# Optimization experiments

Measured on AMD Instinct MI355X. Metric: run time of the kernel, lower is better.

The kernel has to match this reference:

```python
import jax, jax.numpy as jnp
import numpy as np

B = 16384
D = 1024
NG = 64
H = 2  # num_heads = len(conv_kernel_sizes)


def setup_inputs() -> dict:
    key = jax.random.key(0)
    ks = jax.random.split(key, 12)
    s = 0.02
    return {
        "x": jax.random.normal(ks[0], (B, D), jnp.float32),
        "group_labels": jax.random.randint(ks[1], (B,), 0, NG, dtype=jnp.int32),
        "num_groups": NG,
        "conv_w2": jax.random.normal(ks[2], (2,), jnp.float32) * s,
        "conv_b2": jax.random.normal(ks[3], (), jnp.float32) * s,
        "conv_w4": jax.random.normal(ks[4], (4,), jnp.float32) * s,
        "conv_b4": jax.random.normal(ks[5], (), jnp.float32) * s,
        "intra_in_w": jax.random.normal(ks[6], (3 * D, D), jnp.float32) * s,
        "intra_in_b": jnp.zeros((3 * D,), jnp.float32),
        "intra_out_w": jax.random.normal(ks[7], (D, D), jnp.float32) * s,
        "intra_out_b": jnp.zeros((D,), jnp.float32),
        "inter_in_w": jax.random.normal(ks[8], (3 * D, D), jnp.float32) * s,
        "inter_in_b": jnp.zeros((3 * D,), jnp.float32),
        "inter_out_w": jax.random.normal(ks[9], (D, D), jnp.float32) * s,
        "inter_out_b": jnp.zeros((D,), jnp.float32),
        "lin_w": jax.random.normal(ks[10], (D, D), jnp.float32) * s,
        "lin_b": jnp.zeros((D,), jnp.float32),
    }


def _seg_conv(x_s, l_s, w, b):
    """Per-group Conv2d(1,1,(k,1),padding=(k//2,0)) along the group-sorted axis,
    with zero padding at group boundaries and output trimmed to group size.
    out[i] = sum_j w[j] * x[i + j - k//2] if same group else 0."""
    n = x_s.shape[0]
    k = w.shape[0]
    pad = k // 2
    xp = jnp.pad(x_s, ((pad, pad), (0, 0)))
    lp = jnp.pad(l_s, (pad, pad), constant_values=-1)
    out = jnp.zeros_like(x_s)
    for j in range(k):  # k <= 4, static
        m = (lp[j:j + n] == l_s)[:, None]
        out = out + w[j] * jnp.where(m, xp[j:j + n], 0.0)
    return out + b


def _mha_self(xs, in_w, in_b, out_w, out_b, h):
    """torch nn.MultiheadAttention self-attention, seq-first xs: [S, N, D]."""
    S, N, Dm = xs.shape
    dh = Dm // h
    qkv = jnp.einsum('snd,ed->sne', xs, in_w) + in_b
    q, k, v = jnp.split(qkv, 3, axis=-1)
    q = q.reshape(S, N, h, dh)
    k = k.reshape(S, N, h, dh)
    v = v.reshape(S, N, h, dh)
    scores = jnp.einsum('qnhd,knhd->nhqk', q, k) / np.float32(np.sqrt(dh))
    a = jax.nn.softmax(scores, axis=-1)
    o = jnp.einsum('nhqk,knhd->qnhd', a, v).reshape(S, N, Dm)
    return jnp.einsum('snd,ed->sne', o, out_w) + out_b


def reference(x, group_labels, num_groups, conv_w2, conv_b2, conv_w4, conv_b4,
              intra_in_w, intra_in_b, intra_out_w, intra_out_b,
              inter_in_w, inter_in_b, inter_out_w, inter_out_b, lin_w, lin_b):
    n, d = x.shape
    labels = group_labels.astype(jnp.int32)
    perm = jnp.argsort(labels)  # stable: preserves original order within groups
    x_s = x[perm]
    l_s = labels[perm]

    # per-group convs -> [2, N, D] token stack (seq-first for MHA)
    t2 = _seg_conv(x_s, l_s, conv_w2, conv_b2)
    t4 = _seg_conv(x_s, l_s, conv_w4, conv_b4)
    tok = jnp.stack([t2, t4], axis=0)

    # intra attention over the 2 conv tokens per position, mean, then Linear
    intra = _mha_self(tok, intra_in_w, intra_in_b, intra_out_w, intra_out_b, H).mean(axis=0)
    lin_out = intra @ lin_w.T + lin_b  # [N, D]

    # inter-group: seq-len-1 attention over FIRST row of each other group ==
    # out_proj(v_proj(first_row)); mean over the other present groups.
    counts = jax.ops.segment_sum(jnp.ones((n,), jnp.int32), labels, num_segments=num_groups)
    present = counts > 0
    first_idx = jax.ops.segment_min(jnp.arange(n), labels, num_segments=num_groups)
    first_rows = x[jnp.where(present, first_idx, 0)]  # [NG, D]
    Wv = inter_in_w[2 * d:]
    bv = inter_in_b[2 * d:]
    f = (first_rows @ Wv.T + bv) @ inter_out_w.T + inter_out_b  # [NG, D]
    f = jnp.where(present[:, None], f, 0.0)
    n_present = jnp.sum(present.astype(jnp.int32))
    denom = jnp.maximum(n_present - 1, 1).astype(x.dtype)
    inter_mean = (jnp.sum(f, axis=0)[None, :] - f) / denom
    inter_mean = inter_mean * (n_present > 1).astype(x.dtype)

    out_s = lin_out + inter_mean[l_s]
    return jnp.zeros_like(x).at[perm].set(out_s)
```

## Files before the change

### kernel.cpp

```cpp
#include <hip/hip_runtime.h>
#include <hip/hip_bf16.h>

#define B_N 16384
#define D_DIM 1024
#define NGRP 64
#define NCHUNK 64
#define CHUNK 256

typedef __attribute__((ext_vector_type(8))) short short8;
typedef __attribute__((ext_vector_type(8))) unsigned short ushort8;
typedef __attribute__((ext_vector_type(4))) unsigned short ushort4v;
typedef __attribute__((ext_vector_type(4))) float floatx4;

__device__ __forceinline__ float bf2f(unsigned short h) {
    union { unsigned u; float f; } c; c.u = ((unsigned)h) << 16; return c.f;
}
__device__ __forceinline__ unsigned short f2bf(float f) {
    union { float f; unsigned u; } c; c.f = f;
    unsigned r = c.u + 0x7FFFu + ((c.u >> 16) & 1u);
    return (unsigned short)(r >> 16);
}

__device__ __forceinline__ void gload_lds16(const void* g, void* l) {
    __builtin_amdgcn_global_load_lds(
        (const __attribute__((address_space(1))) unsigned int*)g,
        (__attribute__((address_space(3))) unsigned int*)l, 16, 0, 0);
}

__global__ __launch_bounds__(256) void k_hist(const int* __restrict__ labels,
                                              int* __restrict__ hist) {
    __shared__ int lh[NGRP];
    int t = threadIdx.x, c = blockIdx.x;
    if (t < NGRP) lh[t] = 0;
    __syncthreads();
    int lab = labels[c * CHUNK + t];
    atomicAdd(&lh[lab], 1);
    __syncthreads();
    if (t < NGRP) hist[c * NGRP + t] = lh[t];
}

__global__ void k_scan(int* __restrict__ hist, int* __restrict__ gstart,
                       int* __restrict__ counts, float* __restrict__ scal) {
    __shared__ int cnt[NGRP];
    __shared__ int st[NGRP + 1];
    int g = threadIdx.x;
    int run = 0;
    for (int c = 0; c < NCHUNK; c++) {
        int v = hist[c * NGRP + g];
        hist[c * NGRP + g] = run;
        run += v;
    }
    cnt[g] = run;
    counts[g] = run;
    __syncthreads();
    if (g == 0) {
        int s = 0, np = 0;
        for (int i = 0; i < NGRP; i++) { st[i] = s; s += cnt[i]; np += (cnt[i] > 0); }
        st[NGRP] = s;
        scal[0] = (np > 1) ? 1.0f / (float)(np - 1) : 0.0f;
    }
    __syncthreads();
    gstart[g] = st[g];
    if (g == 0) gstart[NGRP] = st[NGRP];
    for (int c = 0; c < NCHUNK; c++) hist[c * NGRP + g] += st[g];
}

__global__ __launch_bounds__(256) void k_scatter(const int* __restrict__ labels,
                                                 const int* __restrict__ hist,
                                                 int* __restrict__ perm,
                                                 int* __restrict__ ls) {
    __shared__ int lab[CHUNK];
    int c = blockIdx.x, t = threadIdx.x;
    int i = c * CHUNK + t;
    int L = labels[i];
    lab[t] = L;
    __syncthreads();
    int rank = 0;
    for (int j = 0; j < t; j++) rank += (lab[j] == L);
    int pos = hist[c * NGRP + L] + rank;
    perm[pos] = i;
    ls[pos] = L;
}

__global__ __launch_bounds__(256) void k_conv(const float* __restrict__ x,
                                              const int* __restrict__ perm,
                                              const int* __restrict__ ls,
                                              const float* __restrict__ w2, const float* __restrict__ b2,
                                              const float* __restrict__ w4, const float* __restrict__ b4,
                                              unsigned short* __restrict__ tok, int c0, int Bc) {
    const int il = blockIdx.x;
    const int i = c0 + il;
    const int li = ls[i];
    const int p0 = perm[i];
    const int pm1 = (i >= 1 && ls[i - 1] == li) ? perm[i - 1] : -1;
    const int pm2 = (i >= 2 && ls[i - 2] == li) ? perm[i - 2] : -1;
    const int pp1 = (i + 1 < B_N && ls[i + 1] == li) ? perm[i + 1] : -1;
    const int c = threadIdx.x * 4;
    floatx4 z = (floatx4)0.0f;
    floatx4 x0 = *(const floatx4*)(x + (size_t)p0 * D_DIM + c);
    floatx4 xm1 = (pm1 >= 0) ? *(const floatx4*)(x + (size_t)pm1 * D_DIM + c) : z;
    floatx4 xm2 = (pm2 >= 0) ? *(const floatx4*)(x + (size_t)pm2 * D_DIM + c) : z;
    floatx4 xp1 = (pp1 >= 0) ? *(const floatx4*)(x + (size_t)pp1 * D_DIM + c) : z;
    const float w20 = w2[0], w21 = w2[1], cb2 = b2[0];
    const float w40 = w4[0], w41 = w4[1], w42 = w4[2], w43 = w4[3], cb4 = b4[0];
    ushort4v o2, o4;
#pragma unroll
    for (int j = 0; j < 4; j++) {
        float t2 = w20 * xm1[j] + w21 * x0[j] + cb2;
        float t4 = w40 * xm2[j] + w41 * xm1[j] + w42 * x0[j] + w43 * xp1[j] + cb4;
        o2[j] = f2bf(t2);
        o4[j] = f2bf(t4);
    }
    *(ushort4v*)(tok + (size_t)il * D_DIM + c) = o2;
    *(ushort4v*)(tok + (size_t)(Bc + il) * D_DIM + c) = o4;
}

__global__ __launch_bounds__(256) void k_prep(const float* __restrict__ intra_in_w,
                                              const float* __restrict__ lin_w,
                                              const float* __restrict__ intra_out_w,
                                              unsigned short* __restrict__ W1b,
                                              unsigned short* __restrict__ linwb,
                                              unsigned short* __restrict__ WoT) {
    __shared__ float tile[32][33];
    const int bx = blockIdx.x;
    if (bx < 4096) {
        int i = bx * 256 + threadIdx.x;
        const float* src;
        unsigned short* dst;
        int j;
        if (i < 786432) { src = intra_in_w; dst = W1b; j = i; }
        else { src = lin_w; dst = linwb; j = i - 786432; }
        floatx4 v = *(const floatx4*)(src + (size_t)j * 4);
        ushort4v o;
#pragma unroll
        for (int q = 0; q < 4; q++) o[q] = f2bf(v[q]);
        *(ushort4v*)(dst + (size_t)j * 4) = o;
    } else {
        const int tb = bx - 4096;
        const int bX = (tb & 31) * 32, bY = (tb >> 5) * 32;
        const int tx = threadIdx.x & 31, ty = threadIdx.x >> 5;
        for (int r = ty; r < 32; r += 8)
            tile[r][tx] = intra_out_w[(size_t)(bY + r) * D_DIM + bX + tx];
        __syncthreads();
        for (int r = ty; r < 32; r += 8)
            WoT[(size_t)(bX + r) * D_DIM + bY + tx] = f2bf(tile[tx][r]);
    }
}

__global__ __launch_bounds__(256) void k_u(const float* __restrict__ x,
                                           const int* __restrict__ perm,
                                           const int* __restrict__ gstart,
                                           const int* __restrict__ counts,
                                           const float* __restrict__ Wfull,
                                           const float* __restrict__ bfull,
                                           float* __restrict__ u,
                                           const float* __restrict__ lin_w,
                                           const float* __restrict__ lin_b,
                                           const float* __restrict__ ob,
                                           float* __restrict__ biasc) {
    const int g = blockIdx.y;
    const int n = blockIdx.x * 256 + threadIdx.x;
    __shared__ __align__(16) float xr[D_DIM];
    const bool isb = (g == NGRP);
    int row = 0;
    if (!isb) {
        const int cnt = counts[g];
        row = (cnt > 0) ? perm[gstart[g]] : 0;
    }
    for (int k = threadIdx.x; k < D_DIM; k += 256)
        xr[k] = isb ? ob[k] : x[(size_t)row * D_DIM + k];
    __syncthreads();
    const float* wrow = isb ? (lin_w + (size_t)n * D_DIM)
                            : (Wfull + (size_t)(2 * D_DIM + n) * D_DIM);
    const floatx4* wr4 = (const floatx4*)wrow;
    const floatx4* xr4 = (const floatx4*)xr;
    float s = isb ? lin_b[n] : bfull[2 * D_DIM + n];
    for (int k4 = 0; k4 < D_DIM / 4; k4++) {
        floatx4 a = xr4[k4], b = wr4[k4];
        s += a[0] * b[0] + a[1] * b[1] + a[2] * b[2] + a[3] * b[3];
    }
    if (isb) biasc[n] = s;
    else u[g * D_DIM + n] = s;
}

__global__ __launch_bounds__(256) void k_f(const float* __restrict__ u,
                                           const int* __restrict__ counts,
                                           const float* __restrict__ W,
                                           const float* __restrict__ b,
                                           float* __restrict__ f) {
    const int g = blockIdx.y;
    const int n = blockIdx.x * 256 + threadIdx.x;
    __shared__ __align__(16) float ur[D_DIM];
    const int cnt = counts[g];
    for (int k = threadIdx.x; k < D_DIM; k += 256) ur[k] = u[g * D_DIM + k];
    __syncthreads();
    const floatx4* wr4 = (const floatx4*)(W + (size_t)n * D_DIM);
    const floatx4* ur4 = (const floatx4*)ur;
    float s = b[n];
    for (int k4 = 0; k4 < D_DIM / 4; k4++) {
        floatx4 a = ur4[k4], w = wr4[k4];
        s += a[0] * w[0] + a[1] * w[1] + a[2] * w[2] + a[3] * w[3];
    }
    f[g * D_DIM + n] = (cnt > 0) ? s : 0.0f;
}

__global__ __launch_bounds__(256) void k_imean(const float* __restrict__ f,
                                               const float* __restrict__ scal,
                                               float* __restrict__ im) {
    int c = blockIdx.x * 256 + threadIdx.x;
    float s = 0.0f;
    for (int g = 0; g < NGRP; g++) s += f[g * D_DIM + c];
    float fl = scal[0];
    for (int g = 0; g < NGRP; g++) im[g * D_DIM + c] = (s - f[g * D_DIM + c]) * fl;
}

template <int MODE>
__global__ __launch_bounds__(256)
void gemm_bt(const unsigned short* __restrict__ A,
             const unsigned short* __restrict__ W,
             int M, int N, int K,
             const float* __restrict__ bias,
             unsigned short* __restrict__ outb,
             float* __restrict__ outf,
             const int* __restrict__ perm,
             const int* __restrict__ ls,
             const float* __restrict__ imean,
             int mhstride, int ldc, int rowoff) {
    __shared__ __align__(16) unsigned short sA[128 * 64];
    __shared__ __align__(16) unsigned short sB[128 * 64];
    const int t = threadIdx.x;
    const int lane = t & 63, wv = t >> 6;
    int bx = blockIdx.x, by = blockIdx.y;
    const int nX = gridDim.x, nY = gridDim.y;
    if ((nY & 7) == 0) {
        const int bid = by * nX + bx;
        const int xcd = bid & 7, j = bid >> 3;
        const int stripe = nY >> 3;
        by = xcd * stripe + j / nX;
        bx = j % nX;
    }
    const int m0 = by * 128, n0 = bx * 128;
    if (MODE == 3) A += (size_t)(n0 >> 9) * (size_t)mhstride;
    const int wm = (wv & 1) * 64, wn = (wv >> 1) * 64;
    const int l15 = lane & 15, quad = lane >> 4;
    const int sw = l15 & 7;

    floatx4 acc[4][4];
#pragma unroll
    for (int i = 0; i < 4; i++)
#pragma unroll
        for (int j = 0; j < 4; j++) acc[i][j] = (floatx4)0.0f;

    for (int k0 = 0; k0 < K; k0 += 64) {
#pragma unroll
        for (int r = 0; r < 4; r++) {
            const int chunk = r * 256 + wv * 64;
            const int idx = chunk + lane;
            const int row = idx >> 3;
            const int kb = (idx & 7) ^ (row & 7);
            gload_lds16(A + (size_t)(m0 + row) * K + k0 + kb * 8, &sA[chunk * 8]);
            gload_lds16(W + (size_t)(n0 + row) * K + k0 + kb * 8, &sB[chunk * 8]);
        }
        __syncthreads();
#pragma unroll
        for (int kk = 0; kk < 64; kk += 32) {
            const int kc = kk >> 3;
            short8 av[4], bv[4];
#pragma unroll
            for (int mt = 0; mt < 4; mt++)
                av[mt] = *(const short8*)&sA[(wm + mt * 16 + l15) * 64 +
                                             (((kc + quad) ^ sw) << 3)];
#pragma unroll
            for (int nt = 0; nt < 4; nt++)
                bv[nt] = *(const short8*)&sB[(wn + nt * 16 + l15) * 64 +
                                             (((kc + quad) ^ sw) << 3)];
#pragma unroll
            for (int mt = 0; mt < 4; mt++)
#pragma unroll
                for (int nt = 0; nt < 4; nt++)
                    acc[mt][nt] = __builtin_amdgcn_mfma_f32_16x16x32_bf16(
                        av[mt], bv[nt], acc[mt][nt], 0, 0, 0);
        }
        __syncthreads();
    }

    if (MODE != 2) {
        const int ld = (MODE == 3) ? ldc : N;
        const int rb = (MODE == 3) ? rowoff : 0;
#pragma unroll
        for (int nt = 0; nt < 4; nt++) {
            const int gc = n0 + wn + nt * 16 + l15;
            const float bb = (MODE == 1) ? 0.0f : bias[gc];
#pragma unroll
            for (int mt = 0; mt < 4; mt++) {
                const int gr = m0 + wm + mt * 16 + quad * 4;
#pragma unroll
                for (int r = 0; r < 4; r++)
                    outb[(size_t)(rb + gr + r) * ld + gc] = f2bf(acc[mt][nt][r] + bb);
            }
        }
    } else {
        float bb[4];
        int gc4[4];
#pragma unroll
        for (int nt = 0; nt < 4; nt++) {
            gc4[nt] = n0 + wn + nt * 16 + l15;
            bb[nt] = bias[gc4[nt]];
        }
#pragma unroll
        for (int mt = 0; mt < 4; mt++) {
#pragma unroll
            for (int r = 0; r < 4; r++) {
                const int i = m0 + wm + mt * 16 + quad * 4 + r;
                const int orow = perm[i];
                const int lg = ls[i];
#pragma unroll
                for (int nt = 0; nt < 4; nt++)
                    outf[(size_t)orow * N + gc4[nt]] =
                        acc[mt][nt][r] + bb[nt] + imean[lg * D_DIM + gc4[nt]];
            }
        }
    }
}

__global__ __launch_bounds__(256) void k_score(const unsigned short* __restrict__ qk,
                                               floatx4* __restrict__ gam, int Bc) {
    const int t = threadIdx.x;
    const int lane = t & 63, wv = t >> 6;
    const int bl = blockIdx.x * 4 + wv;
    const unsigned short* r2 = qk + (size_t)bl * 2048;
    const unsigned short* r4 = qk + (size_t)(Bc + bl) * 2048;
    float cw[4];
#pragma unroll
    for (int h = 0; h < 2; h++) {
        const int off = h * 512 + lane * 8;
        short8 q2 = *(const short8*)(r2 + off);
        short8 q4 = *(const short8*)(r4 + off);
        short8 k2 = *(const short8*)(r2 + 1024 + off);
        short8 k4 = *(const short8*)(r4 + 1024 + off);
        float s22 = 0, s24 = 0, s42 = 0, s44 = 0;
#pragma unroll
        for (int j = 0; j < 8; j++) {
            float q2f = bf2f((unsigned short)q2[j]), q4f = bf2f((unsigned short)q4[j]);
            float k2f = bf2f((unsigned short)k2[j]), k4f = bf2f((unsigned short)k4[j]);
            s22 += q2f * k2f; s24 += q2f * k4f; s42 += q4f * k2f; s44 += q4f * k4f;
        }
#pragma unroll
        for (int d = 32; d > 0; d >>= 1) {
            s22 += __shfl_xor(s22, d, 64);
            s24 += __shfl_xor(s24, d, 64);
            s42 += __shfl_xor(s42, d, 64);
            s44 += __shfl_xor(s44, d, 64);
        }
        const float sc = 0.044194173824159216f;
        s22 *= sc; s24 *= sc; s42 *= sc; s44 *= sc;
        float m0 = fmaxf(s22, s24), e22 = __expf(s22 - m0), e24 = __expf(s24 - m0);
        float w24 = e24 / (e22 + e24), w22 = 1.0f - w24;
        float m1 = fmaxf(s42, s44), e42 = __expf(s42 - m1), e44 = __expf(s44 - m1);
        float w44 = e44 / (e42 + e44), w42 = 1.0f - w44;
        cw[h * 2 + 0] = 0.5f * (w22 + w42);
        cw[h * 2 + 1] = 0.5f * (w24 + w44);
    }
    if (lane == 0) {
        floatx4 g;
        g[0] = cw[0]; g[1] = cw[1]; g[2] = cw[2]; g[3] = cw[3];
        gam[bl] = g;
    }
}

__global__ __launch_bounds__(256) void k_zprep(const unsigned short* __restrict__ tok,
                                               const floatx4* __restrict__ gam,
                                               unsigned short* __restrict__ z, int Bc) {
    const int idx = blockIdx.x * 256 + threadIdx.x;
    const int bl = idx >> 7;
    const int seg = (idx & 127) * 8;
    floatx4 g = gam[bl];
    short8 a = *(const short8*)(tok + (size_t)bl * D_DIM + seg);
    short8 b = *(const short8*)(tok + (size_t)(Bc + bl) * D_DIM + seg);
    ushort8 z1, z2;
#pragma unroll
    for (int j = 0; j < 8; j++) {
        float af = bf2f((unsigned short)a[j]), bf = bf2f((unsigned short)b[j]);
        z1[j] = f2bf(g[0] * af + g[1] * bf);
        z2[j] = f2bf(g[2] * af + g[3] * bf);
    }
    *(ushort8*)(z + (size_t)bl * D_DIM + seg) = z1;
    *(ushort8*)(z + (size_t)(Bc + bl) * D_DIM + seg) = z2;
}

extern "C" void kernel_launch(void* const* d_in, const int* in_sizes, int n_in,
                              void* d_out, int out_size, void* d_ws, size_t ws_size,
                              hipStream_t stream) {
    const float* x = (const float*)d_in[0];
    const int* labels = (const int*)d_in[1];
    const float* conv_w2 = (const float*)d_in[3];
    const float* conv_b2 = (const float*)d_in[4];
    const float* conv_w4 = (const float*)d_in[5];
    const float* conv_b4 = (const float*)d_in[6];
    const float* intra_in_w = (const float*)d_in[7];
    const float* intra_in_b = (const float*)d_in[8];
    const float* intra_out_w = (const float*)d_in[9];
    const float* intra_out_b = (const float*)d_in[10];
    const float* inter_in_w = (const float*)d_in[11];
    const float* inter_in_b = (const float*)d_in[12];
    const float* inter_out_w = (const float*)d_in[13];
    const float* inter_out_b = (const float*)d_in[14];
    const float* lin_w = (const float*)d_in[15];
    const float* lin_b = (const float*)d_in[16];
    float* out = (float*)d_out;

    char* p = (char*)d_ws;
    auto alloc = [&](size_t bytes) -> void* {
        void* r = (void*)p;
        p += (bytes + 255) & ~(size_t)255;
        return r;
    };
    int* perm = (int*)alloc(B_N * 4);
    int* lss = (int*)alloc(B_N * 4);
    int* hist = (int*)alloc(NCHUNK * NGRP * 4);
    int* gstart = (int*)alloc((NGRP + 1) * 4);
    int* counts = (int*)alloc(NGRP * 4);
    float* scal = (float*)alloc(4);
    unsigned short* om = (unsigned short*)alloc((size_t)B_N * D_DIM * 2);
    unsigned short* W1b = (unsigned short*)alloc((size_t)3 * D_DIM * D_DIM * 2);
    unsigned short* linwb = (unsigned short*)alloc((size_t)D_DIM * D_DIM * 2);
    unsigned short* WoT = (unsigned short*)alloc((size_t)D_DIM * D_DIM * 2);
    unsigned short* Wc = (unsigned short*)alloc((size_t)D_DIM * D_DIM * 2);
    float* u = (float*)alloc((size_t)NGRP * D_DIM * 4);
    float* fbuf = (float*)alloc((size_t)NGRP * D_DIM * 4);
    float* imean = (float*)alloc((size_t)NGRP * D_DIM * 4);
    float* biasc = (float*)alloc(D_DIM * 4);

    size_t used = (size_t)(p - (char*)d_ws);
    size_t remain = (ws_size > used) ? (ws_size - used) : 0;
    int Bc = 512;
    const int cand[6] = {16384, 8192, 4096, 2048, 1024, 512};
    for (int ci = 0; ci < 6; ci++) {
        if ((size_t)16400 * cand[ci] + 8192 <= remain) { Bc = cand[ci]; break; }
    }
    unsigned short* tokc = (unsigned short*)alloc((size_t)2 * Bc * D_DIM * 2);
    unsigned short* qkc = (unsigned short*)alloc((size_t)2 * Bc * 2 * D_DIM * 2);
    unsigned short* zc = (unsigned short*)alloc((size_t)2 * Bc * D_DIM * 2);
    floatx4* gam = (floatx4*)alloc((size_t)Bc * 16);

    k_hist<<<NCHUNK, CHUNK, 0, stream>>>(labels, hist);
    k_scan<<<1, NGRP, 0, stream>>>(hist, gstart, counts, scal);
    k_scatter<<<NCHUNK, CHUNK, 0, stream>>>(labels, hist, perm, lss);
    k_prep<<<4096 + 1024, 256, 0, stream>>>(intra_in_w, lin_w, intra_out_w, W1b, linwb, WoT);
    gemm_bt<1><<<dim3(8, 8), 256, 0, stream>>>(linwb, WoT, 1024, 1024, 1024, nullptr, Wc,
                                               nullptr, nullptr, nullptr, nullptr, 0, 0, 0);
    k_u<<<dim3(4, NGRP + 1), 256, 0, stream>>>(x, perm, gstart, counts, inter_in_w,
                                               inter_in_b, u, lin_w, lin_b, intra_out_b,
                                               biasc);
    k_f<<<dim3(4, NGRP), 256, 0, stream>>>(u, counts, inter_out_w, inter_out_b, fbuf);
    k_imean<<<4, 256, 0, stream>>>(fbuf, scal, imean);
    const int nchunks = B_N / Bc;
    for (int c = 0; c < nchunks; c++) {
        const int c0 = c * Bc;
        k_conv<<<Bc, 256, 0, stream>>>(x, perm, lss, conv_w2, conv_b2, conv_w4, conv_b4,
                                       tokc, c0, Bc);
        gemm_bt<0><<<dim3(16, 2 * Bc / 128), 256, 0, stream>>>(
            tokc, W1b, 2 * Bc, 2 * D_DIM, D_DIM, intra_in_b, qkc, nullptr, nullptr,
            nullptr, nullptr, 0, 0, 0);
        k_score<<<Bc / 4, 256, 0, stream>>>(qkc, gam, Bc);
        k_zprep<<<Bc / 2, 256, 0, stream>>>(tokc, gam, zc, Bc);
        gemm_bt<3><<<dim3(8, Bc / 128), 256, 0, stream>>>(
            zc, W1b + (size_t)2 * D_DIM * D_DIM, Bc, D_DIM, D_DIM,
            intra_in_b + 2 * D_DIM, om, nullptr, nullptr, nullptr, nullptr,
            Bc * D_DIM, D_DIM, c0);
    }
    gemm_bt<2><<<dim3(8, 128), 256, 0, stream>>>(om, Wc, B_N, D_DIM, D_DIM, biasc, nullptr,
                                                 out, perm, lss, imean, 0, 0, 0);
}
```

Measured before the change: 649.2 us.

## Fold V projection into combined output weight and fuse QK projection with scoring

The value projection, out-projection and final linear are precomputed into one combined weight GG, with the V bias folded through as well. This removes the per-chunk V GEMM and the intermediate om buffer, so the final GEMM reads the interleaved z tokens directly with K=2048. Q and K projections are fused into one kernel that reduces the per-token dot products in registers and accumulates scores with atomics, so the full QK activation is never written out. The chunking loop is dropped in favour of full-batch buffers. In exchange there are extra weight-side GEMMs, atomic contention on the scores buffer, and a larger workspace requirement.

After: 952.6 us. +46.7%, slower.

```diff
diff --git a/kernel.cpp b/kernel.cpp
--- a/kernel.cpp
+++ b/kernel.cpp
@@ -87,9 +87,8 @@
                                               const int* __restrict__ ls,
                                               const float* __restrict__ w2, const float* __restrict__ b2,
                                               const float* __restrict__ w4, const float* __restrict__ b4,
-                                              unsigned short* __restrict__ tok, int c0, int Bc) {
-    const int il = blockIdx.x;
-    const int i = c0 + il;
+                                              unsigned short* __restrict__ tok) {
+    const int i = blockIdx.x;
     const int li = ls[i];
     const int p0 = perm[i];
     const int pm1 = (i >= 1 && ls[i - 1] == li) ? perm[i - 1] : -1;
@@ -111,40 +110,60 @@
         o2[j] = f2bf(t2);
         o4[j] = f2bf(t4);
     }
-    *(ushort4v*)(tok + (size_t)il * D_DIM + c) = o2;
-    *(ushort4v*)(tok + (size_t)(Bc + il) * D_DIM + c) = o4;
+    *(ushort4v*)(tok + (size_t)(2 * i) * D_DIM + c) = o2;
+    *(ushort4v*)(tok + (size_t)(2 * i + 1) * D_DIM + c) = o4;
 }
 
 __global__ __launch_bounds__(256) void k_prep(const float* __restrict__ intra_in_w,
                                               const float* __restrict__ lin_w,
                                               const float* __restrict__ intra_out_w,
-                                              unsigned short* __restrict__ W1b,
+                                              unsigned short* __restrict__ Wqk,
                                               unsigned short* __restrict__ linwb,
-                                              unsigned short* __restrict__ WoT) {
+                                              unsigned short* __restrict__ WoT,
+                                              unsigned short* __restrict__ WvT) {
     __shared__ float tile[32][33];
     const int bx = blockIdx.x;
-    if (bx < 4096) {
+    if (bx < 3072) {
         int i = bx * 256 + threadIdx.x;
         const float* src;
         unsigned short* dst;
         int j;
-        if (i < 786432) { src = intra_in_w; dst = W1b; j = i; }
-        else { src = lin_w; dst = linwb; j = i - 786432; }
+        if (i < 524288) { src = intra_in_w; dst = Wqk; j = i; }
+        else { src = lin_w; dst = linwb; j = i - 524288; }
         floatx4 v = *(const floatx4*)(src + (size_t)j * 4);
         ushort4v o;
 #pragma unroll
         for (int q = 0; q < 4; q++) o[q] = f2bf(v[q]);
         *(ushort4v*)(dst + (size_t)j * 4) = o;
     } else {
-        const int tb = bx - 4096;
+        int tb = bx - 3072;
+        const float* src;
+        unsigned short* dst;
+        if (tb < 1024) { src = intra_out_w; dst = WoT; }
+        else { src = intra_in_w + (size_t)2048 * D_DIM; dst = WvT; tb -= 1024; }
         const int bX = (tb & 31) * 32, bY = (tb >> 5) * 32;
         const int tx = threadIdx.x & 31, ty = threadIdx.x >> 5;
         for (int r = ty; r < 32; r += 8)
-            tile[r][tx] = intra_out_w[(size_t)(bY + r) * D_DIM + bX + tx];
+            tile[r][tx] = src[(size_t)(bY + r) * D_DIM + bX + tx];
         __syncthreads();
         for (int r = ty; r < 32; r += 8)
-            WoT[(size_t)(bX + r) * D_DIM + bY + tx] = f2bf(tile[tx][r]);
-    }
+            dst[(size_t)(bX + r) * D_DIM + bY + tx] = f2bf(tile[tx][r]);
+    }
+}
+
+__global__ __launch_bounds__(256) void k_ob2(const float* __restrict__ ow,
+                                             const float* __restrict__ ob,
+                                             const float* __restrict__ bv,
+                                             float* __restrict__ ob2) {
+    int e = blockIdx.x * 256 + threadIdx.x;
+    const floatx4* wr4 = (const floatx4*)(ow + (size_t)e * D_DIM);
+    const floatx4* bv4 = (const floatx4*)bv;
+    float s = ob[e];
+    for (int k4 = 0; k4 < D_DIM / 4; k4++) {
+        floatx4 a = wr4[k4], b = bv4[k4];
+        s += a[0] * b[0] + a[1] * b[1] + a[2] * b[2] + a[3] * b[3];
+    }
+    ob2[e] = s;
 }
 
 __global__ __launch_bounds__(256) void k_u(const float* __restrict__ x,
@@ -156,7 +175,7 @@
                                            float* __restrict__ u,
                                            const float* __restrict__ lin_w,
                                            const float* __restrict__ lin_b,
-                                           const float* __restrict__ ob,
+                                           const float* __restrict__ ob2,
                                            float* __restrict__ biasc) {
     const int g = blockIdx.y;
     const int n = blockIdx.x * 256 + threadIdx.x;
@@ -168,7 +187,7 @@
         row = (cnt > 0) ? perm[gstart[g]] : 0;
     }
     for (int k = threadIdx.x; k < D_DIM; k += 256)
-        xr[k] = isb ? ob[k] : x[(size_t)row * D_DIM + k];
+        xr[k] = isb ? ob2[k] : x[(size_t)row * D_DIM + k];
     __syncthreads();
     const float* wrow = isb ? (lin_w + (size_t)n * D_DIM)
                             : (Wfull + (size_t)(2 * D_DIM + n) * D_DIM);
@@ -214,18 +233,21 @@
     for (int g = 0; g < NGRP; g++) im[g * D_DIM + c] = (s - f[g * D_DIM + c]) * fl;
 }
 
+__global__ __launch_bounds__(256) void k_zero(float* __restrict__ p) {
+    ((floatx4*)p)[blockIdx.x * 256 + threadIdx.x] = (floatx4)0.0f;
+}
+
 template <int MODE>
 __global__ __launch_bounds__(256)
 void gemm_bt(const unsigned short* __restrict__ A,
              const unsigned short* __restrict__ W,
-             int M, int N, int K,
+             int M, int N, int K, int lda, int ldw,
              const float* __restrict__ bias,
-             unsigned short* __restrict__ outb,
+             unsigned short* __restrict__ outb, int ldc,
              float* __restrict__ outf,
              const int* __restrict__ perm,
              const int* __restrict__ ls,
-             const float* __restrict__ imean,
-             int mhstride, int ldc, int rowoff) {
+             const float* __restrict__ imean) {
     __shared__ __align__(16) unsigned short sA[128 * 64];
     __shared__ __align__(16) unsigned short sB[128 * 64];
     const int t = threadIdx.x;
@@ -240,7 +262,6 @@
         bx = j % nX;
     }
     const int m0 = by * 128, n0 = bx * 128;
-    if (MODE == 3) A += (size_t)(n0 >> 9) * (size_t)mhstride;
     const int wm = (wv & 1) * 64, wn = (wv >> 1) * 64;
     const int l15 = lane & 15, quad = lane >> 4;
     const int sw = l15 & 7;
@@ -258,8 +279,8 @@
             const int idx = chunk + lane;
             const int row = idx >> 3;
             const int kb = (idx & 7) ^ (row & 7);
-            gload_lds16(A + (size_t)(m0 + row) * K + k0 + kb * 8, &sA[chunk * 8]);
-            gload_lds16(W + (size_t)(n0 + row) * K + k0 + kb * 8, &sB[chunk * 8]);
+            gload_lds16(A + (size_t)(m0 + row) * lda + k0 + kb * 8, &sA[chunk * 8]);
+            gload_lds16(W + (size_t)(n0 + row) * ldw + k0 + kb * 8, &sB[chunk * 8]);
         }
         __syncthreads();
 #pragma unroll
@@ -284,19 +305,16 @@
         __syncthreads();
     }
 
-    if (MODE != 2) {
-        const int ld = (MODE == 3) ? ldc : N;
-        const int rb = (MODE == 3) ? rowoff : 0;
+    if (MODE == 1) {
 #pragma unroll
         for (int nt = 0; nt < 4; nt++) {
             const int gc = n0 + wn + nt * 16 + l15;
-            const float bb = (MODE == 1) ? 0.0f : bias[gc];
 #pragma unroll
             for (int mt = 0; mt < 4; mt++) {
                 const int gr = m0 + wm + mt * 16 + quad * 4;
 #pragma unroll
                 for (int r = 0; r < 4; r++)
-                    outb[(size_t)(rb + gr + r) * ld + gc] = f2bf(acc[mt][nt][r] + bb);
+                    outb[(size_t)(gr + r) * ldc + gc] = f2bf(acc[mt][nt][r]);
             }
         }
     } else {
@@ -323,60 +341,152 @@
     }
 }
 
-__global__ __launch_bounds__(256) void k_score(const unsigned short* __restrict__ qk,
-                                               floatx4* __restrict__ gam, int Bc) {
+__global__ __launch_bounds__(256) void k_qkscore(const unsigned short* __restrict__ A,
+                                                 const unsigned short* __restrict__ Wq,
+                                                 const unsigned short* __restrict__ Wk,
+                                                 const float* __restrict__ bq,
+                                                 const float* __restrict__ bk,
+                                                 float* __restrict__ scores) {
+    __shared__ __align__(16) unsigned short sA[128 * 64];
+    __shared__ __align__(16) unsigned short sBq[64 * 64];
+    __shared__ __align__(16) unsigned short sBk[64 * 64];
     const int t = threadIdx.x;
     const int lane = t & 63, wv = t >> 6;
-    const int bl = blockIdx.x * 4 + wv;
-    const unsigned short* r2 = qk + (size_t)bl * 2048;
-    const unsigned short* r4 = qk + (size_t)(Bc + bl) * 2048;
-    float cw[4];
+    int bx = blockIdx.x, by = blockIdx.y;
+    {
+        const int nX = gridDim.x, nY = gridDim.y;
+        const int bid = by * nX + bx;
+        const int xcd = bid & 7, j = bid >> 3;
+        const int stripe = nY >> 3;
+        by = xcd * stripe + j / nX;
+        bx = j % nX;
+    }
+    const int m0 = by * 128, n0 = bx * 64;
+    const int wm = (wv & 1) * 64, wn = (wv >> 1) * 32;
+    const int l15 = lane & 15, quad = lane >> 4;
+    const int sw = l15 & 7;
+
+    floatx4 qa[4][2], ka[4][2];
+#pragma unroll
+    for (int i = 0; i < 4; i++)
+#pragma unroll
+        for (int j = 0; j < 2; j++) { qa[i][j] = (floatx4)0.0f; ka[i][j] = (floatx4)0.0f; }
+
+    for (int k0 = 0; k0 < D_DIM; k0 += 64) {
+#pragma unroll
+        for (int r = 0; r < 4; r++) {
+            const int chunk = r * 256 + wv * 64;
+            const int idx = chunk + lane;
+            const int row = idx >> 3;
+            const int kb = (idx & 7) ^ (row & 7);
+            gload_lds16(A + (size_t)(m0 + row) * D_DIM + k0 + kb * 8, &sA[chunk * 8]);
+        }
+#pragma unroll
+        for (int r = 0; r < 2; r++) {
+            const int chunk = r * 256 + wv * 64;
+            const int idx = chunk + lane;
+            const int row = idx >> 3;
+            const int kb = (idx & 7) ^ (row & 7);
+            gload_lds16(Wq + (size_t)(n0 + row) * D_DIM + k0 + kb * 8, &sBq[chunk * 8]);
+            gload_lds16(Wk + (size_t)(n0 + row) * D_DIM + k0 + kb * 8, &sBk[chunk * 8]);
+        }
+        __syncthreads();
+#pragma unroll
+        for (int kk = 0; kk < 64; kk += 32) {
+            const int kc = kk >> 3;
+            short8 av[4], bqv[2], bkv[2];
+#pragma unroll
+            for (int mt = 0; mt < 4; mt++)
+                av[mt] = *(const short8*)&sA[(wm + mt * 16 + l15) * 64 +
+                                             (((kc + quad) ^ sw) << 3)];
+#pragma unroll
+            for (int nt = 0; nt < 2; nt++) {
+                bqv[nt] = *(const short8*)&sBq[(wn + nt * 16 + l15) * 64 +
+                                               (((kc + quad) ^ sw) << 3)];
+                bkv[nt] = *(const short8*)&sBk[(wn + nt * 16 + l15) * 64 +
+                                               (((kc + quad) ^ sw) << 3)];
+            }
+#pragma unroll
+            for (int mt = 0; mt < 4; mt++)
+#pragma unroll
+                for (int nt = 0; nt < 2; nt++) {
+                    qa[mt][nt] = __builtin_amdgcn_mfma_f32_16x16x32_bf16(
+                        av[mt], bqv[nt], qa[mt][nt], 0, 0, 0);
+                    ka[mt][nt] = __builtin_amdgcn_mfma_f32_16x16x32_bf16(
+                        av[mt], bkv[nt], ka[mt][nt], 0, 0, 0);
+                }
+        }
+        __syncthreads();
+    }
+
+    const int head = n0 >> 9;
+    float bqv2[2], bkv2[2];
+#pragma unroll
+    for (int nt = 0; nt < 2; nt++) {
+        const int col = n0 + wn + nt * 16 + l15;
+        bqv2[nt] = bq[col];
+        bkv2[nt] = bk[col];
+    }
+#pragma unroll
+    for (int mt = 0; mt < 4; mt++) {
+#pragma unroll
+        for (int p = 0; p < 2; p++) {
+            float s22 = 0, s24 = 0, s42 = 0, s44 = 0;
+#pragma unroll
+            for (int nt = 0; nt < 2; nt++) {
+                float q0 = qa[mt][nt][2 * p] + bqv2[nt];
+                float q1 = qa[mt][nt][2 * p + 1] + bqv2[nt];
+                float k0v = ka[mt][nt][2 * p] + bkv2[nt];
+                float k1v = ka[mt][nt][2 * p + 1] + bkv2[nt];
+                s22 += q0 * k0v; s24 += q0 * k1v; s42 += q1 * k0v; s44 += q1 * k1v;
+            }
+#pragma unroll
+            for (int d = 1; d < 16; d <<= 1) {
+                s22 += __shfl_xor(s22, d, 64);
+                s24 += __shfl_xor(s24, d, 64);
+                s42 += __shfl_xor(s42, d, 64);
+                s44 += __shfl_xor(s44, d, 64);
+            }
+            if (l15 == 0) {
+                const int i = (m0 + wm + mt * 16 + quad * 4 + 2 * p) >> 1;
+                atomicAdd(&scores[i * 8 + head * 4 + 0], s22);
+                atomicAdd(&scores[i * 8 + head * 4 + 1], s24);
+                atomicAdd(&scores[i * 8 + head * 4 + 2], s42);
+                atomicAdd(&scores[i * 8 + head * 4 + 3], s44);
+            }
+        }
+    }
+}
+
+__global__ __launch_bounds__(256) void k_gam(const float* __restrict__ scores,
+                                             floatx4* __restrict__ gam) {
+    const int i = blockIdx.x * 256 + threadIdx.x;
+    const float sc = 0.044194173824159216f;
+    floatx4 g;
 #pragma unroll
     for (int h = 0; h < 2; h++) {
-        const int off = h * 512 + lane * 8;
-        short8 q2 = *(const short8*)(r2 + off);
-        short8 q4 = *(const short8*)(r4 + off);
-        short8 k2 = *(const short8*)(r2 + 1024 + off);
-        short8 k4 = *(const short8*)(r4 + 1024 + off);
-        float s22 = 0, s24 = 0, s42 = 0, s44 = 0;
-#pragma unroll
-        for (int j = 0; j < 8; j++) {
-            float q2f = bf2f((unsigned short)q2[j]), q4f = bf2f((unsigned short)q4[j]);
-            float k2f = bf2f((unsigned short)k2[j]), k4f = bf2f((unsigned short)k4[j]);
-            s22 += q2f * k2f; s24 += q2f * k4f; s42 += q4f * k2f; s44 += q4f * k4f;
-        }
-#pragma unroll
-        for (int d = 32; d > 0; d >>= 1) {
-            s22 += __shfl_xor(s22, d, 64);
-            s24 += __shfl_xor(s24, d, 64);
-            s42 += __shfl_xor(s42, d, 64);
-            s44 += __shfl_xor(s44, d, 64);
-        }
-        const float sc = 0.044194173824159216f;
-        s22 *= sc; s24 *= sc; s42 *= sc; s44 *= sc;
+        float s22 = scores[i * 8 + h * 4 + 0] * sc;
+        float s24 = scores[i * 8 + h * 4 + 1] * sc;
+        float s42 = scores[i * 8 + h * 4 + 2] * sc;
+        float s44 = scores[i * 8 + h * 4 + 3] * sc;
         float m0 = fmaxf(s22, s24), e22 = __expf(s22 - m0), e24 = __expf(s24 - m0);
         float w24 = e24 / (e22 + e24), w22 = 1.0f - w24;
         float m1 = fmaxf(s42, s44), e42 = __expf(s42 - m1), e44 = __expf(s44 - m1);
         float w44 = e44 / (e42 + e44), w42 = 1.0f - w44;
-        cw[h * 2 + 0] = 0.5f * (w22 + w42);
-        cw[h * 2 + 1] = 0.5f * (w24 + w44);
-    }
-    if (lane == 0) {
-        floatx4 g;
-        g[0] = cw[0]; g[1] = cw[1]; g[2] = cw[2]; g[3] = cw[3];
-        gam[bl] = g;
-    }
-}
-
-__global__ __launch_bounds__(256) void k_zprep(const unsigned short* __restrict__ tok,
-                                               const floatx4* __restrict__ gam,
-                                               unsigned short* __restrict__ z, int Bc) {
+        g[h * 2 + 0] = 0.5f * (w22 + w42);
+        g[h * 2 + 1] = 0.5f * (w24 + w44);
+    }
+    gam[i] = g;
+}
+
+__global__ __launch_bounds__(256) void k_zprep(unsigned short* __restrict__ tok,
+                                               const floatx4* __restrict__ gam) {
     const int idx = blockIdx.x * 256 + threadIdx.x;
-    const int bl = idx >> 7;
+    const int i = idx >> 7;
     const int seg = (idx & 127) * 8;
-    floatx4 g = gam[bl];
-    short8 a = *(const short8*)(tok + (size_t)bl * D_DIM + seg);
-    short8 b = *(const short8*)(tok + (size_t)(Bc + bl) * D_DIM + seg);
+    floatx4 g = gam[i];
+    short8 a = *(const short8*)(tok + (size_t)(2 * i) * D_DIM + seg);
+    short8 b = *(const short8*)(tok + (size_t)(2 * i + 1) * D_DIM + seg);
     ushort8 z1, z2;
 #pragma unroll
     for (int j = 0; j < 8; j++) {
@@ -384,8 +494,8 @@
         z1[j] = f2bf(g[0] * af + g[1] * bf);
         z2[j] = f2bf(g[2] * af + g[3] * bf);
     }
-    *(ushort8*)(z + (size_t)bl * D_DIM + seg) = z1;
-    *(ushort8*)(z + (size_t)(Bc + bl) * D_DIM + seg) = z2;
+    *(ushort8*)(tok + (size_t)(2 * i) * D_DIM + seg) = z1;
+    *(ushort8*)(tok + (size_t)(2 * i + 1) * D_DIM + seg) = z2;
 }
 
 extern "C" void kernel_launch(void* const* d_in, const int* in_sizes, int n_in,
@@ -421,54 +531,46 @@
     int* gstart = (int*)alloc((NGRP + 1) * 4);
     int* counts = (int*)alloc(NGRP * 4);
     float* scal = (float*)alloc(4);
-    unsigned short* om = (unsigned short*)alloc((size_t)B_N * D_DIM * 2);
-    unsigned short* W1b = (unsigned short*)alloc((size_t)3 * D_DIM * D_DIM * 2);
+    unsigned short* tok = (unsigned short*)alloc((size_t)2 * B_N * D_DIM * 2);
+    unsigned short* Wqk = (unsigned short*)alloc((size_t)2 * D_DIM * D_DIM * 2);
     unsigned short* linwb = (unsigned short*)alloc((size_t)D_DIM * D_DIM * 2);
     unsigned short* WoT = (unsigned short*)alloc((size_t)D_DIM * D_DIM * 2);
+    unsigned short* WvT = (unsigned short*)alloc((size_t)D_DIM * D_DIM * 2);
     unsigned short* Wc = (unsigned short*)alloc((size_t)D_DIM * D_DIM * 2);
+    unsigned short* GG = (unsigned short*)alloc((size_t)D_DIM * 2 * D_DIM * 2);
+    float* scores = (float*)alloc((size_t)B_N * 8 * 4);
+    floatx4* gam = (floatx4*)alloc((size_t)B_N * 16);
     float* u = (float*)alloc((size_t)NGRP * D_DIM * 4);
     float* fbuf = (float*)alloc((size_t)NGRP * D_DIM * 4);
     float* imean = (float*)alloc((size_t)NGRP * D_DIM * 4);
     float* biasc = (float*)alloc(D_DIM * 4);
-
-    size_t used = (size_t)(p - (char*)d_ws);
-    size_t remain = (ws_size > used) ? (ws_size - used) : 0;
-    int Bc = 512;
-    const int cand[6] = {16384, 8192, 4096, 2048, 1024, 512};
-    for (int ci = 0; ci < 6; ci++) {
-        if ((size_t)16400 * cand[ci] + 8192 <= remain) { Bc = cand[ci]; break; }
-    }
-    unsigned short* tokc = (unsigned short*)alloc((size_t)2 * Bc * D_DIM * 2);
-    unsigned short* qkc = (unsigned short*)alloc((size_t)2 * Bc * 2 * D_DIM * 2);
-    unsigned short* zc = (unsigned short*)alloc((size_t)2 * Bc * D_DIM * 2);
-    floatx4* gam = (floatx4*)alloc((size_t)Bc * 16);
+    float* ob2 = (float*)alloc(D_DIM * 4);
 
     k_hist<<<NCHUNK, CHUNK, 0, stream>>>(labels, hist);
     k_scan<<<1, NGRP, 0, stream>>>(hist, gstart, counts, scal);
     k_scatter<<<NCHUNK, CHUNK, 0, stream>>>(labels, hist, perm, lss);
-    k_prep<<<4096 + 1024, 256, 0, stream>>>(intra_in_w, lin_w, intra_out_w, W1b, linwb, WoT);
-    gemm_bt<1><<<dim3(8, 8), 256, 0, stream>>>(linwb, WoT, 1024, 1024, 1024, nullptr, Wc,
-                                               nullptr, nullptr, nullptr, nullptr, 0, 0, 0);
+    k_prep<<<3072 + 2048, 256, 0, stream>>>(intra_in_w, lin_w, intra_out_w, Wqk, linwb,
+                                            WoT, WvT);
+    gemm_bt<1><<<dim3(8, 8), 256, 0, stream>>>(linwb, WoT, 1024, 1024, 1024, 1024, 1024,
+                                               nullptr, Wc, 1024, nullptr, nullptr,
+                                               nullptr, nullptr);
+    gemm_bt<1><<<dim3(8, 8), 256, 0, stream>>>(Wc, WvT, 1024, 1024, 512, 1024, 1024,
+                                               nullptr, GG, 2048, nullptr, nullptr,
+                                               nullptr, nullptr);
+    gemm_bt<1><<<dim3(8, 8), 256, 0, stream>>>(Wc + 512, WvT + 512, 1024, 1024, 512, 1024,
+                                               1024, nullptr, GG + 1024, 2048, nullptr,
+                                               nullptr, nullptr, nullptr);
+    k_ob2<<<4, 256, 0, stream>>>(intra_out_w, intra_out_b, intra_in_b + 2 * D_DIM, ob2);
     k_u<<<dim3(4, NGRP + 1), 256, 0, stream>>>(x, perm, gstart, counts, inter_in_w,
-                                               inter_in_b, u, lin_w, lin_b, intra_out_b,
-                                               biasc);
+                                               inter_in_b, u, lin_w, lin_b, ob2, biasc);
     k_f<<<dim3(4, NGRP), 256, 0, stream>>>(u, counts, inter_out_w, inter_out_b, fbuf);
     k_imean<<<4, 256, 0, stream>>>(fbuf, scal, imean);
-    const int nchunks = B_N / Bc;
-    for (int c = 0; c < nchunks; c++) {
-        const int c0 = c * Bc;
-        k_conv<<<Bc, 256, 0, stream>>>(x, perm, lss, conv_w2, conv_b2, conv_w4, conv_b4,
-                                       tokc, c0, Bc);
-        gemm_bt<0><<<dim3(16, 2 * Bc / 128), 256, 0, stream>>>(
-            tokc, W1b, 2 * Bc, 2 * D_DIM, D_DIM, intra_in_b, qkc, nullptr, nullptr,
-            nullptr, nullptr, 0, 0, 0);
-        k_score<<<Bc / 4, 256, 0, stream>>>(qkc, gam, Bc);
-        k_zprep<<<Bc / 2, 256, 0, stream>>>(tokc, gam, zc, Bc);
-        gemm_bt<3><<<dim3(8, Bc / 128), 256, 0, stream>>>(
-            zc, W1b + (size_t)2 * D_DIM * D_DIM, Bc, D_DIM, D_DIM,
-            intra_in_b + 2 * D_DIM, om, nullptr, nullptr, nullptr, nullptr,
-            Bc * D_DIM, D_DIM, c0);
-    }
-    gemm_bt<2><<<dim3(8, 128), 256, 0, stream>>>(om, Wc, B_N, D_DIM, D_DIM, biasc, nullptr,
-                                                 out, perm, lss, imean, 0, 0, 0);
-}
+    k_conv<<<B_N, 256, 0, stream>>>(x, perm, lss, conv_w2, conv_b2, conv_w4, conv_b4, tok);
+    k_zero<<<B_N * 8 / 1024, 256, 0, stream>>>(scores);
+    k_qkscore<<<dim3(16, 256), 256, 0, stream>>>(tok, Wqk, Wqk + (size_t)D_DIM * D_DIM,
+                                                 intra_in_b, intra_in_b + D_DIM, scores);
+    k_gam<<<B_N / 256, 256, 0, stream>>>(scores, gam);
+    k_zprep<<<B_N / 2, 256, 0, stream>>>(tok, gam);
+    gemm_bt<2><<<dim3(8, 128), 256, 0, stream>>>(tok, GG, B_N, 1024, 2048, 2048, 2048,
+                                                 biasc, nullptr, 0, out, perm, lss, imean);
+}
```
